# Optimization experiments

Measured on AMD Instinct MI355X. Metric: run time of the kernel, lower is better.

## Reference

```python
import jax, jax.numpy as jnp
import numpy as np
from functools import partial

DIM = 25
LAYERS = 10
NCLS = 7


def setup_inputs() -> dict:
    key = jax.random.key(0)
    ks = jax.random.split(key, 10)
    T, B = 2048, 512
    s = 1.0 / np.sqrt(DIM)  # pytorch LSTM init scale
    x = jax.random.normal(ks[0], (T, B, DIM), dtype=jnp.float32)
    h0 = jax.random.normal(ks[1], (LAYERS, B, DIM), dtype=jnp.float32)
    c0 = jax.random.normal(ks[2], (LAYERS, B, DIM), dtype=jnp.float32)
    W_ih = jax.random.uniform(ks[3], (LAYERS, 4 * DIM, DIM), minval=-s, maxval=s, dtype=jnp.float32)
    W_hh = jax.random.uniform(ks[4], (LAYERS, 4 * DIM, DIM), minval=-s, maxval=s, dtype=jnp.float32)
    # b = b_ih + b_hh combined (they always appear summed)
    b = jax.random.uniform(ks[5], (LAYERS, 4 * DIM), minval=-2 * s, maxval=2 * s, dtype=jnp.float32)
    fc_w = jax.random.uniform(ks[6], (NCLS, DIM), minval=-s, maxval=s, dtype=jnp.float32)
    fc_b = jax.random.uniform(ks[7], (NCLS,), minval=-s, maxval=s, dtype=jnp.float32)
    return {"x": x, "h0": h0, "c0": c0, "W_ih": W_ih, "W_hh": W_hh, "b": b,
            "fc_w": fc_w, "fc_b": fc_b}


def _lstm_stack(x, h0, c0, W_ih, W_hh, b):
    # x: [T,B,D]; h0,c0: [L,B,D]; W_ih,W_hh: [L,4D,D]; b: [L,4D]
    def step(carry, xt):
        h, c = carry  # each [L,B,D]
        inp = xt
        hs, cs = [], []
        for l in range(LAYERS):
            gates = inp @ W_ih[l].T + h[l] @ W_hh[l].T + b[l]  # [B,4D]
            i, f, g, o = jnp.split(gates, 4, axis=-1)  # torch gate order i,f,g,o
            i = jax.nn.sigmoid(i)
            f = jax.nn.sigmoid(f)
            g = jnp.tanh(g)
            o = jax.nn.sigmoid(o)
            cl = f * c[l] + i * g
            hl = o * jnp.tanh(cl)
            hs.append(hl)
            cs.append(cl)
            inp = hl
        return (jnp.stack(hs), jnp.stack(cs)), inp

    (_, _), out = jax.lax.scan(step, (h0, c0), x)
    return out  # [T,B,D] top-layer hidden states


def reference(x, h0, c0, W_ih, W_hh, b, fc_w, fc_b):
    out = _lstm_stack(x, h0, c0, W_ih, W_hh, b)  # [T,B,D]
    y = out.reshape(-1, DIM) @ fc_w.T + fc_b  # [T*B,7]
    return jax.nn.softmax(y, axis=-1)
```

## Files before the change

### kernel.cpp

```cpp
#include <hip/hip_runtime.h>

#define TT 2048
#define BQ 512
#define LAYERS 10
#define NC 7
#define CH 8
#define NCH (TT / CH)

#define E_S 16
#define C_S (2 * E_S)
#define S_S (CH * C_S)
#define P_S ((LAYERS + 1) * S_S)

typedef _Float16 half2v __attribute__((ext_vector_type(2)));
typedef _Float16 f16x8 __attribute__((ext_vector_type(8)));
typedef float f32x4 __attribute__((ext_vector_type(4)));

__device__ __forceinline__ float sigm(float z) {
  return __builtin_amdgcn_rcpf(1.0f + __expf(-z));
}
__device__ __forceinline__ float dot2(unsigned w, unsigned v, float acc) {
  return __builtin_amdgcn_fdot2(__builtin_bit_cast(half2v, w),
                                __builtin_bit_cast(half2v, v), acc, false);
}
__device__ __forceinline__ unsigned pkh2(float a, float b) {
  union { _Float16 h[2]; unsigned u; } z;
  z.h[0] = (_Float16)a; z.h[1] = (_Float16)b;
  return z.u;
}

#define LOAD13(dst, src)                             \
  do {                                               \
    *(uint4*)&(dst)[0] = *(const uint4*)((src) + 0); \
    *(uint4*)&(dst)[4] = *(const uint4*)((src) + 4); \
    *(uint4*)&(dst)[8] = *(const uint4*)((src) + 8); \
    (dst)[12] = (src)[12];                           \
  } while (0)

__launch_bounds__(768, 3)
__global__ void lstm_fused(const float* __restrict__ x,
                           const float* __restrict__ h0,
                           const float* __restrict__ c0,
                           const float* __restrict__ Wih,
                           const float* __restrict__ Whh,
                           const float* __restrict__ bias,
                           const float* __restrict__ fcw,
                           const float* __restrict__ fcb,
                           float* __restrict__ out) {
  __shared__ __align__(16) unsigned hs[2 * P_S];
  __shared__ float eb[2][CH][8];

  const int tid = threadIdx.x;
  const int w = tid >> 6;
  const int lane = tid & 63;
  const int b0 = blockIdx.x * 2;
  const int n15 = lane & 15;
  const int q4 = lane >> 4;
  const int arb = (n15 & 1) * E_S + 4 * q4;
  const bool lay = (w < LAYERS);
  const int q4e = q4 & 1;
  const bool q4hi = (q4 >= 2);
  const int u = (q4hi ? 16 : 0) + n15;
  const bool av = lay && (!q4hi || (n15 < 9));
  const bool isfc = (w >= LAYERS) && (lane < 7 * CH);
  const int efc = w - LAYERS;
  const int jg = lane / 7;
  const int cls = lane - jg * 7;

  f16x8 BX[8], BH[8];
  unsigned Wf[13];
  float bb[4] = {0.f, 0.f, 0.f, 0.f};
  float bf = 0.f;
  float c = 0.f;

  const int sgg = lane / 13;
  const int li = lane - sgg * 13;
  const int jb = sgg * 4;
  const int i0 = 2 * li;
  const int i1 = (li < 12) ? (2 * li + 1) : 0;
  const bool stg = (w >= LAYERS) && (lane < 26);
  float xA[4], xB[4];
#pragma unroll
  for (int jj = 0; jj < 4; ++jj) { xA[jj] = 0.f; xB[jj] = 0.f; }

  for (int i = tid; i < 2 * P_S; i += 768) hs[i] = 0u;

  if (lay) {
#pragma unroll
    for (int nt = 0; nt < 8; ++nt) {
      const int g = nt & 3;
      const int uu = ((nt >> 2) ? 16 : 0) + n15;
      const bool gok = (uu < 25);
      const int row = 25 * g + (gok ? uu : 0);
      const float* px = Wih + (w * 100 + row) * 25;
      const float* ph = Whh + (w * 100 + row) * 25;
#pragma unroll
      for (int d = 0; d < 4; ++d) {
        const int k0 = 8 * q4 + 2 * d, k1 = k0 + 1;
        float x0 = 0.f, x1 = 0.f, h0v = 0.f, h1v = 0.f;
        if (gok && k0 < 25) { x0 = px[k0]; h0v = ph[k0]; }
        if (gok && k1 < 25) { x1 = px[k1]; h1v = ph[k1]; }
        BX[nt][2 * d]     = (_Float16)x0;
        BX[nt][2 * d + 1] = (_Float16)x1;
        BH[nt][2 * d]     = (_Float16)h0v;
        BH[nt][2 * d + 1] = (_Float16)h1v;
      }
    }
    if (av) {
#pragma unroll
      for (int g = 0; g < 4; ++g) bb[g] = bias[w * 100 + 25 * g + u];
      c = c0[(w * BQ + b0 + q4e) * 25 + u];
    }
  } else if (isfc) {
    const float* pf = fcw + cls * 25;
#pragma unroll
    for (int k = 0; k < 13; ++k) {
      const int k0 = 2 * k, k1 = 2 * k + 1;
      Wf[k] = pkh2(pf[k0], (k1 < 25) ? pf[k1] : 0.f);
    }
    bf = fcb[cls];
  }
  __syncthreads();

  if (av) {
    const float h00 = h0[(w * BQ + b0 + q4e) * 25 + u];
    _Float16* hp = (_Float16*)(hs + ((w & 1) ^ 1) * P_S + (w + 1) * S_S +
                               (CH - 1) * C_S);
    hp[q4e * 32 + u] = (_Float16)h00;
  }

  if (stg) {
#pragma unroll
    for (int jj = 0; jj < 4; ++jj) {
      const float* p = x + ((size_t)(jb + jj) * BQ + (b0 + efc)) * 25;
      hs[1 * P_S + (jb + jj) * C_S + efc * E_S + li] =
          pkh2(p[i0], (li < 12) ? p[i1] : 0.f);
    }
#pragma unroll
    for (int jj = 0; jj < 4; ++jj) {
      const float* p = x + ((size_t)(CH + jb + jj) * BQ + (b0 + efc)) * 25;
      xA[jj] = p[i0];
      xB[jj] = (li < 12) ? p[i1] : 0.f;
    }
  }
  __syncthreads();

  for (int m = 0; m < NCH + LAYERS; ++m) {
    const int pr = (m & 1) ^ 1;
    const int pw = m & 1;

    if (lay) {
      const int mc = m - w;
      if ((unsigned)mc < (unsigned)NCH) {
        const unsigned* islot = hs + pr * P_S + w * S_S + arb;
        const unsigned* o0p =
            hs + pr * P_S + (w + 1) * S_S + (CH - 1) * C_S + arb;
        unsigned* ob = hs + pw * P_S + (w + 1) * S_S;
        const unsigned* obr = ob + arb;

#pragma unroll
        for (int j = 0; j < CH; ++j) {
          const f16x8 ax =
              __builtin_bit_cast(f16x8, *(const uint4*)(islot + j * C_S));
          const uint4 ahu = (j == 0) ? *(const uint4*)o0p
                                     : *(const uint4*)(obr + (j - 1) * C_S);
          const f16x8 ah = __builtin_bit_cast(f16x8, ahu);
          f32x4 Cr[8];
#pragma unroll
          for (int nt = 0; nt < 8; ++nt) {
            f32x4 z4 = {0.f, 0.f, 0.f, 0.f};
            z4 = __builtin_amdgcn_mfma_f32_16x16x32_f16(ax, BX[nt], z4,
                                                        0, 0, 0);
            Cr[nt] = __builtin_amdgcn_mfma_f32_16x16x32_f16(ah, BH[nt], z4,
                                                            0, 0, 0);
          }
          if (av) {
            const float vi = q4hi ? (q4e ? Cr[4][1] : Cr[4][0])
                                  : (q4e ? Cr[0][1] : Cr[0][0]);
            const float vf = q4hi ? (q4e ? Cr[5][1] : Cr[5][0])
                                  : (q4e ? Cr[1][1] : Cr[1][0]);
            const float vg = q4hi ? (q4e ? Cr[6][1] : Cr[6][0])
                                  : (q4e ? Cr[2][1] : Cr[2][0]);
            const float vo = q4hi ? (q4e ? Cr[7][1] : Cr[7][0])
                                  : (q4e ? Cr[3][1] : Cr[3][0]);
            const float gi = sigm(vi + bb[0]);
            const float gf = sigm(vf + bb[1]);
            const float pg = vg + bb[2];
            const float gg = 2.0f * sigm(2.0f * pg) - 1.0f;
            const float go = sigm(vo + bb[3]);
            c = gf * c + gi * gg;
            const float th = 2.0f * sigm(2.0f * c) - 1.0f;
            const float hv = go * th;
            _Float16* hp = (_Float16*)(ob + j * C_S);
            hp[q4e * 32 + u] = (_Float16)hv;
          }
        }
      }
    } else {
      if (stg) {
        if (m + 1 < NCH) {
#pragma unroll
          for (int jj = 0; jj < 4; ++jj) {
            hs[pw * P_S + (jb + jj) * C_S + efc * E_S + li] =
                pkh2(xA[jj], xB[jj]);
          }
        }
        if (m + 2 < NCH) {
          const size_t tb = (size_t)(m + 2) * CH + jb;
#pragma unroll
          for (int jj = 0; jj < 4; ++jj) {
            const float* p = x + ((tb + jj) * BQ + (b0 + efc)) * 25;
            xA[jj] = p[i0];
            xB[jj] = (li < 12) ? p[i1] : 0.f;
          }
        }
      }
      const int mc = m - LAYERS;
      if (isfc && (unsigned)mc < (unsigned)NCH) {
        const unsigned* hp =
            hs + pr * P_S + LAYERS * S_S + jg * C_S + efc * E_S;
        unsigned Hv[13];
        LOAD13(Hv, hp);
        float acc = bf;
#pragma unroll
        for (int k = 0; k < 13; ++k) acc = dot2(Wf[k], Hv[k], acc);
        const float ev = __expf(acc);
        eb[efc][jg][cls] = ev;
        const float ssum = eb[efc][jg][0] + eb[efc][jg][1] + eb[efc][jg][2] +
                           eb[efc][jg][3] + eb[efc][jg][4] + eb[efc][jg][5] +
                           eb[efc][jg][6];
        const int t = mc * CH + jg;
        out[((size_t)t * BQ + (b0 + efc)) * NC + cls] =
            ev * __builtin_amdgcn_rcpf(ssum);
      }
    }
    __syncthreads();
  }
}

extern "C" void kernel_launch(void* const* d_in, const int* in_sizes, int n_in,
                              void* d_out, int out_size, void* d_ws, size_t ws_size,
                              hipStream_t stream) {
  const float* x   = (const float*)d_in[0];
  const float* h0  = (const float*)d_in[1];
  const float* c0  = (const float*)d_in[2];
  const float* Wih = (const float*)d_in[3];
  const float* Whh = (const float*)d_in[4];
  const float* b   = (const float*)d_in[5];
  const float* fcw = (const float*)d_in[6];
  const float* fcb = (const float*)d_in[7];
  float* out = (float*)d_out;

  lstm_fused<<<dim3(256), dim3(768), 0, stream>>>(x, h0, c0, Wih, Whh, b, fcw,
                                                  fcb, out);
}
```

Before: 1.245 ms.

## Batch input projection for whole chunk with one MFMA pass before recurrence

Moves the input-to-hidden MFMA out of the per-timestep dependent loop. All CH timesteps of the chunk's inputs (2 batch columns × 8 steps packed into the 16 MFMA rows) are projected with a single set of 8 MFMAs. The results go through a new per-layer LDS scratch buffer and are reloaded as per-step float4 gate contributions. This halves the MFMAs on the serial recurrence path, at the cost of extra LDS space and traffic, more registers, and possible occupancy pressure.

```diff
diff --git a/kernel.cpp b/kernel.cpp
--- a/kernel.cpp
+++ b/kernel.cpp
@@ -11,6 +11,11 @@
 #define C_S (2 * E_S)
 #define S_S (CH * C_S)
 #define P_S ((LAYERS + 1) * S_S)
+
+#define XU 4
+#define XJ (26 * XU)
+#define XE (CH * XJ)
+#define XW (2 * XE)
 
 typedef _Float16 half2v __attribute__((ext_vector_type(2)));
 typedef _Float16 f16x8 __attribute__((ext_vector_type(8)));
@@ -48,6 +53,7 @@
                            const float* __restrict__ fcb,
                            float* __restrict__ out) {
   __shared__ __align__(16) unsigned hs[2 * P_S];
+  __shared__ __align__(16) float xls[LAYERS * XW];
   __shared__ float eb[2][CH][8];
 
   const int tid = threadIdx.x;
@@ -57,6 +63,7 @@
   const int n15 = lane & 15;
   const int q4 = lane >> 4;
   const int arb = (n15 & 1) * E_S + 4 * q4;
+  const int arbx = (n15 & 7) * C_S + (n15 >> 3) * E_S + 4 * q4;
   const bool lay = (w < LAYERS);
   const int q4e = q4 & 1;
   const bool q4hi = (q4 >= 2);
@@ -152,25 +159,50 @@
     if (lay) {
       const int mc = m - w;
       if ((unsigned)mc < (unsigned)NCH) {
-        const unsigned* islot = hs + pr * P_S + w * S_S + arb;
+        const unsigned* islot = hs + pr * P_S + w * S_S;
         const unsigned* o0p =
             hs + pr * P_S + (w + 1) * S_S + (CH - 1) * C_S + arb;
         unsigned* ob = hs + pw * P_S + (w + 1) * S_S;
         const unsigned* obr = ob + arb;
+        float* xw = xls + w * XW;
+
+        {
+          const f16x8 axc =
+              __builtin_bit_cast(f16x8, *(const uint4*)(islot + arbx));
+          const f32x4 z4 = {0.f, 0.f, 0.f, 0.f};
+#pragma unroll
+          for (int nt = 0; nt < 8; ++nt) {
+            const f32x4 Cx =
+                __builtin_amdgcn_mfma_f32_16x16x32_f16(axc, BX[nt], z4,
+                                                       0, 0, 0);
+            const int g = nt & 3;
+            const int uu = ((nt >> 2) ? 16 : 0) + n15;
+            if (uu < 25) {
+#pragma unroll
+              for (int rr = 0; rr < 4; ++rr) {
+                const int row = 4 * q4 + rr;
+                xw[(row >> 3) * XE + (row & 7) * XJ + uu * XU + g] = Cx[rr];
+              }
+            }
+          }
+        }
+        f32x4 xs[CH];
+        if (av) {
+#pragma unroll
+          for (int j = 0; j < CH; ++j) {
+            xs[j] = *(const f32x4*)(xw + q4e * XE + j * XJ + u * XU);
+          }
+        }
 
 #pragma unroll
         for (int j = 0; j < CH; ++j) {
-          const f16x8 ax =
-              __builtin_bit_cast(f16x8, *(const uint4*)(islot + j * C_S));
           const uint4 ahu = (j == 0) ? *(const uint4*)o0p
                                      : *(const uint4*)(obr + (j - 1) * C_S);
           const f16x8 ah = __builtin_bit_cast(f16x8, ahu);
+          const f32x4 z4 = {0.f, 0.f, 0.f, 0.f};
           f32x4 Cr[8];
 #pragma unroll
           for (int nt = 0; nt < 8; ++nt) {
-            f32x4 z4 = {0.f, 0.f, 0.f, 0.f};
-            z4 = __builtin_amdgcn_mfma_f32_16x16x32_f16(ax, BX[nt], z4,
-                                                        0, 0, 0);
             Cr[nt] = __builtin_amdgcn_mfma_f32_16x16x32_f16(ah, BH[nt], z4,
                                                             0, 0, 0);
           }
@@ -183,11 +215,11 @@
                                   : (q4e ? Cr[2][1] : Cr[2][0]);
             const float vo = q4hi ? (q4e ? Cr[7][1] : Cr[7][0])
                                   : (q4e ? Cr[3][1] : Cr[3][0]);
-            const float gi = sigm(vi + bb[0]);
-            const float gf = sigm(vf + bb[1]);
-            const float pg = vg + bb[2];
+            const float gi = sigm(vi + xs[j][0] + bb[0]);
+            const float gf = sigm(vf + xs[j][1] + bb[1]);
+            const float pg = vg + xs[j][2] + bb[2];
             const float gg = 2.0f * sigm(2.0f * pg) - 1.0f;
-            const float go = sigm(vo + bb[3]);
+            const float go = sigm(vo + xs[j][3] + bb[3]);
             c = gf * c + gi * gg;
             const float th = 2.0f * sigm(2.0f * c) - 1.0f;
             const float hv = go * th;
```

Result: no change. 1.267 ms (+1.8%).
